# Performance work log

Measured on AMD Instinct MI355X. Metric: run time of the kernel, lower is better.

Reference implementation:

```python
import jax, jax.numpy as jnp
import numpy as np

N_NODES = 50000
N_EDGES = 1600000
D_IN = 64
D_EDGE = 64
DIMS = [128, 128, 128]  # atom_embedding_sizes
N_GRAPHS = 64


def setup_inputs() -> dict:
    key = jax.random.key(0)
    ks = jax.random.split(key, 4 + 4 * len(DIMS))
    inp = {
        "x": jax.random.normal(ks[0], (N_NODES, D_IN), dtype=jnp.float32),
        "edge_index": jax.random.randint(ks[1], (2, N_EDGES), 0, N_NODES),
        "edge_attr": jax.random.uniform(ks[2], (N_EDGES, D_EDGE), dtype=jnp.float32),
        "batch": jnp.sort(jax.random.randint(ks[3], (N_NODES,), 0, N_GRAPHS)),
    }
    in_dim = D_IN
    ki = 4
    for l, out_dim in enumerate(DIMS):
        se = 1.0 / np.sqrt(in_dim + D_EDGE)
        sr = 1.0 / np.sqrt(in_dim)
        inp[f"We{l}"] = jax.random.uniform(ks[ki + 0], (in_dim + D_EDGE, out_dim), jnp.float32, -se, se)
        inp[f"be{l}"] = jnp.zeros((out_dim,), jnp.float32)
        inp[f"Wr{l}"] = jax.random.uniform(ks[ki + 1], (in_dim, out_dim), jnp.float32, -sr, sr)
        inp[f"br{l}"] = jnp.zeros((out_dim,), jnp.float32)
        ki += 2
        in_dim = out_dim
    return inp


def reference(x, edge_index, edge_attr, batch,
              We0, be0, Wr0, br0,
              We1, be1, Wr1, br1,
              We2, be2, Wr2, br2):
    params = [(We0, be0, Wr0, br0), (We1, be1, Wr1, br1), (We2, be2, Wr2, br2)]
    src, dst = edge_index[0], edge_index[1]  # PyG convention: messages flow src -> dst
    for We, be, Wr, br in params:
        # ESAGEConv: message = Linear([x_j || edge_attr]); add-aggregate to dst;
        # root transform Linear(x_i); then ReLU (module activation).
        msg = jnp.concatenate([x[src], edge_attr], axis=-1) @ We + be  # [E, out]
        aggr = jax.ops.segment_sum(msg, dst, num_segments=N_NODES)     # [N, out]
        x = jax.nn.relu(aggr + x @ Wr + br)
    # readout_pooling='add' -> global_add_pool over graph ids
    return jax.ops.segment_sum(x, batch, num_segments=N_GRAPHS)  # [G, out]
```

## Files before the change

### kernel.cpp

```cpp
#include <hip/hip_runtime.h>
#include <hip/hip_bf16.h>
#include <cstdint>

typedef __attribute__((ext_vector_type(8))) short short8v;
typedef __attribute__((ext_vector_type(4))) float f32x4;

__device__ __forceinline__ float4 add4(float4 a, float4 b) {
  return make_float4(a.x + b.x, a.y + b.y, a.z + b.z, a.w + b.w);
}
__device__ __forceinline__ float bf2f(unsigned short u) {
  union { unsigned int i; float f; } v; v.i = ((unsigned int)u) << 16; return v.f;
}
__device__ __forceinline__ unsigned short f2bf(float f) {
  union { float f; unsigned int i; } v; v.f = f;
  unsigned int r = v.i + 0x7fff + ((v.i >> 16) & 1);
  return (unsigned short)(r >> 16);
}


__global__ void count_deg_kernel(const int* __restrict__ dst, int* __restrict__ deg, int E) {
  int i = blockIdx.x * blockDim.x + threadIdx.x;
  if (i < E) atomicAdd(&deg[dst[i]], 1);
}

__global__ void block_sum_kernel(const int* __restrict__ deg, int* __restrict__ bsum, int N) {
  int t = threadIdx.x;
  int i = blockIdx.x * 512 + t;
  int v = (i < N) ? deg[i] : 0;
#pragma unroll
  for (int off = 32; off > 0; off >>= 1) v += __shfl_down(v, off, 64);
  __shared__ int ws[8];
  int lane = t & 63, wid = t >> 6;
  if (lane == 0) ws[wid] = v;
  __syncthreads();
  if (t == 0) {
    int s = 0;
#pragma unroll
    for (int j = 0; j < 8; ++j) s += ws[j];
    bsum[blockIdx.x] = s;
  }
}

__global__ void scan_small_kernel(const int* __restrict__ bsum, int* __restrict__ boffs, int B) {
  int t = threadIdx.x;
  int lane = t & 63, wid = t >> 6;
  int v = (t < B) ? bsum[t] : 0;
  int incl = v;
#pragma unroll
  for (int off = 1; off < 64; off <<= 1) {
    int u = __shfl_up(incl, off, 64);
    if (lane >= off) incl += u;
  }
  __shared__ int ws[2];
  if (lane == 63) ws[wid] = incl;
  __syncthreads();
  int base = (wid == 1) ? ws[0] : 0;
  if (t < B) boffs[t] = base + incl - v;
}

__global__ void ptrs_kernel(const int* __restrict__ deg, const int* __restrict__ boffs,
                            int* __restrict__ ptrs, int N) {
  int t = threadIdx.x;
  int i = blockIdx.x * 512 + t;
  int lane = t & 63, wid = t >> 6;
  int v = (i < N) ? deg[i] : 0;
  int incl = v;
#pragma unroll
  for (int off = 1; off < 64; off <<= 1) {
    int u = __shfl_up(incl, off, 64);
    if (lane >= off) incl += u;
  }
  __shared__ int ws[8];
  if (lane == 63) ws[wid] = incl;
  __syncthreads();
  if (t == 0) {
    int s = 0;
#pragma unroll
    for (int j = 0; j < 8; ++j) { int tmp = ws[j]; ws[j] = s; s += tmp; }
  }
  __syncthreads();
  if (i < N) ptrs[i + 1] = boffs[blockIdx.x] + ws[wid] + incl;
  if (i == 0 && blockIdx.x == 0) ptrs[0] = 0;
}

__global__ void fill_csr_kernel(const int* __restrict__ src, const int* __restrict__ dst,
                                const int* __restrict__ ptrs, int* __restrict__ cnt,
                                int2* __restrict__ csr, int E) {
  int i = blockIdx.x * blockDim.x + threadIdx.x;
  if (i < E) {
    int d = dst[i];
    int pos = ptrs[d] + atomicAdd(&cnt[d], 1);
    csr[pos] = make_int2(src[i], i);
  }
}


__global__ void f2bf_stream_kernel(const float* __restrict__ in, unsigned short* __restrict__ out, int n) {
  int i = (blockIdx.x * blockDim.x + threadIdx.x) * 8;
  if (i < n) {
    float4 v0 = *(const float4*)(in + i);
    float4 v1 = *(const float4*)(in + i + 4);
    short8v o;
    o[0] = (short)f2bf(v0.x); o[1] = (short)f2bf(v0.y);
    o[2] = (short)f2bf(v0.z); o[3] = (short)f2bf(v0.w);
    o[4] = (short)f2bf(v1.x); o[5] = (short)f2bf(v1.y);
    o[6] = (short)f2bf(v1.z); o[7] = (short)f2bf(v1.w);
    *(short8v*)(out + i) = o;
  }
}

__global__ void pack_wt_kernel(const float* __restrict__ We, int rowsE,
                               const float* __restrict__ Wr, int Ktot,
                               unsigned short* __restrict__ Wt) {
  int idx = blockIdx.x * blockDim.x + threadIdx.x;
  if (idx >= 128 * Ktot) return;
  int c = idx / Ktot, k = idx % Ktot;
  float v = (k < rowsE) ? We[(size_t)k * 128 + c] : Wr[(size_t)(k - rowsE) * 128 + c];
  Wt[idx] = f2bf(v);
}


__global__ __launch_bounds__(256) void agg_ea_kernel(
    const int* __restrict__ ptrs, const int2* __restrict__ csr,
    const float* __restrict__ ea, unsigned short* __restrict__ agge, int N) {
  int n = blockIdx.x;
  int t = threadIdx.x;
  int slot = t >> 4, cg = t & 15;
  int s = ptrs[n], e = ptrs[n + 1];
  float4 a0 = make_float4(0, 0, 0, 0), a1 = make_float4(0, 0, 0, 0);
  int i = s + slot;
  for (; i + 16 < e; i += 32) {
    int r0 = csr[i].y, r1 = csr[i + 16].y;
    a0 = add4(a0, *((const float4*)(ea + (size_t)r0 * 64) + cg));
    a1 = add4(a1, *((const float4*)(ea + (size_t)r1 * 64) + cg));
  }
  if (i < e) {
    int r0 = csr[i].y;
    a0 = add4(a0, *((const float4*)(ea + (size_t)r0 * 64) + cg));
  }
  a0 = add4(a0, a1);
  __shared__ float red[16][64];
  *reinterpret_cast<float4*>(&red[slot][cg * 4]) = a0;
  __syncthreads();
  if (t < 64) {
    float sum = 0.f;
#pragma unroll
    for (int r = 0; r < 16; ++r) sum += red[r][t];
    agge[(size_t)n * 64 + t] = f2bf(sum);
  }
}

__global__ __launch_bounds__(256) void agg_bf64_kernel(
    const int* __restrict__ ptrs, const int2* __restrict__ csr,
    const unsigned short* __restrict__ xb, unsigned short* __restrict__ outagg, int N) {
  int n = blockIdx.x;
  int t = threadIdx.x;
  int slot = t >> 3, cg = t & 7;
  int s = ptrs[n], e = ptrs[n + 1];
  float a[8];
#pragma unroll
  for (int j = 0; j < 8; ++j) a[j] = 0.f;
  for (int i = s + slot; i < e; i += 32) {
    int r = csr[i].x;
    short8v v = *(const short8v*)(xb + (size_t)r * 64 + cg * 8);
#pragma unroll
    for (int j = 0; j < 8; ++j) a[j] += bf2f((unsigned short)v[j]);
  }
  __shared__ float red[32][64];
#pragma unroll
  for (int j = 0; j < 8; ++j) red[slot][cg * 8 + j] = a[j];
  __syncthreads();
  if (t < 64) {
    float sum = 0.f;
#pragma unroll
    for (int r = 0; r < 32; ++r) sum += red[r][t];
    outagg[(size_t)n * 64 + t] = f2bf(sum);
  }
}

__global__ __launch_bounds__(256) void agg_bf128_kernel(
    const int* __restrict__ ptrs, const int2* __restrict__ csr,
    const unsigned short* __restrict__ xb, unsigned short* __restrict__ outagg, int N) {
  int n = blockIdx.x;
  int t = threadIdx.x;
  int slot = t >> 4, cg = t & 15;
  int s = ptrs[n], e = ptrs[n + 1];
  float a[8];
#pragma unroll
  for (int j = 0; j < 8; ++j) a[j] = 0.f;
  int i = s + slot;
  for (; i + 16 < e; i += 32) {
    int r0 = csr[i].x, r1 = csr[i + 16].x;
    short8v v0 = *(const short8v*)(xb + (size_t)r0 * 128 + cg * 8);
    short8v v1 = *(const short8v*)(xb + (size_t)r1 * 128 + cg * 8);
#pragma unroll
    for (int j = 0; j < 8; ++j) a[j] += bf2f((unsigned short)v0[j]) + bf2f((unsigned short)v1[j]);
  }
  if (i < e) {
    int r0 = csr[i].x;
    short8v v0 = *(const short8v*)(xb + (size_t)r0 * 128 + cg * 8);
#pragma unroll
    for (int j = 0; j < 8; ++j) a[j] += bf2f((unsigned short)v0[j]);
  }
  __shared__ float red[16][128];
#pragma unroll
  for (int j = 0; j < 8; ++j) red[slot][cg * 8 + j] = a[j];
  __syncthreads();
  if (t < 128) {
    float sum = 0.f;
#pragma unroll
    for (int r = 0; r < 16; ++r) sum += red[r][t];
    outagg[(size_t)n * 128 + t] = f2bf(sum);
  }
}

__global__ __launch_bounds__(256) void gemm_mfma_kernel(
    const unsigned short* __restrict__ A1, int w1, int k1,
    const unsigned short* __restrict__ A2, int w2, int k2,
    const unsigned short* __restrict__ A3, int w3, int k3,
    const unsigned short* __restrict__ Wt, int Ktot,
    const float* __restrict__ be, const float* __restrict__ br,
    const int* __restrict__ deg, unsigned short* __restrict__ out, int N) {
  int t = threadIdx.x;
  int wave = t >> 6, lane = t & 63;
  int rit = lane & 15, kgrp = lane >> 4;
  int n0 = blockIdx.x * 64;
  int arow = n0 + wave * 16 + rit;
  if (arow >= N) arow = N - 1;
  f32x4 acc[8];
#pragma unroll
  for (int c = 0; c < 8; ++c) acc[c] = (f32x4){0.f, 0.f, 0.f, 0.f};

  const unsigned short* As[3] = {A1, A2, A3};
  const int wds[3] = {w1, w2, w3};
  const int ks[3] = {k1, k2, k3};
  int kbase = 0;
  for (int s = 0; s < 3; ++s) {
    const unsigned short* Arow = As[s] + (size_t)arow * wds[s] + kgrp * 8;
    int K = ks[s];
    for (int kk = 0; kk < K; kk += 32) {
      short8v a = *(const short8v*)(Arow + kk);
      int kg = kbase + kk + kgrp * 8;
#pragma unroll
      for (int c = 0; c < 8; ++c) {
        short8v b = *(const short8v*)(Wt + (size_t)(c * 16 + rit) * Ktot + kg);
        acc[c] = __builtin_amdgcn_mfma_f32_16x16x32_bf16(a, b, acc[c], 0, 0, 0);
      }
    }
    kbase += K;
  }

  __shared__ unsigned short st[64][136];
  float dg[4];
#pragma unroll
  for (int r = 0; r < 4; ++r) {
    int n = n0 + wave * 16 + kgrp * 4 + r;
    dg[r] = (float)deg[n < N ? n : N - 1];
  }
#pragma unroll
  for (int c = 0; c < 8; ++c) {
    int col = c * 16 + rit;
    float bev = be[col], brv = br[col];
#pragma unroll
    for (int r = 0; r < 4; ++r) {
      float v = acc[c][r] + dg[r] * bev + brv;
      st[wave * 16 + kgrp * 4 + r][col] = f2bf(fmaxf(v, 0.f));
    }
  }
  __syncthreads();
#pragma unroll
  for (int it = 0; it < 4; ++it) {
    int idx = t + it * 256;
    int row = idx >> 4, cg = idx & 15;
    int n = n0 + row;
    if (n < N)
      *(short8v*)(out + (size_t)n * 128 + cg * 8) = *(const short8v*)(&st[row][cg * 8]);
  }
}

__global__ void pool_kernel(const unsigned short* __restrict__ x, const int* __restrict__ batch,
                            float* __restrict__ out, int N) {
  int n0 = blockIdx.x * 128;
  int c = threadIdx.x;
  if (n0 >= N) return;
  int end = min(n0 + 128, N);
  float acc = 0.f;
  int g = batch[n0];
  for (int n = n0; n < end; ++n) {
    int gn = batch[n];
    if (gn != g) {
      atomicAdd(&out[g * 128 + c], acc);
      acc = 0.f;
      g = gn;
    }
    acc += bf2f(x[(size_t)n * 128 + c]);
  }
  atomicAdd(&out[g * 128 + c], acc);
}


extern "C" void kernel_launch(void* const* d_in, const int* in_sizes, int n_in,
                              void* d_out, int out_size, void* d_ws, size_t ws_size,
                              hipStream_t stream) {
  const float* x_in       = (const float*)d_in[0];
  const int*   edge_index = (const int*)d_in[1];
  const float* edge_attr  = (const float*)d_in[2];
  const int*   batch      = (const int*)d_in[3];
  const float* We0 = (const float*)d_in[4];
  const float* be0 = (const float*)d_in[5];
  const float* Wr0 = (const float*)d_in[6];
  const float* br0 = (const float*)d_in[7];
  const float* We1 = (const float*)d_in[8];
  const float* be1 = (const float*)d_in[9];
  const float* Wr1 = (const float*)d_in[10];
  const float* br1 = (const float*)d_in[11];
  const float* We2 = (const float*)d_in[12];
  const float* be2 = (const float*)d_in[13];
  const float* Wr2 = (const float*)d_in[14];
  const float* br2 = (const float*)d_in[15];

  float* out = (float*)d_out;

  int N = in_sizes[0] / 64;
  int E = in_sizes[1] / 2;
  const int* src = edge_index;
  const int* dst = edge_index + E;

  char* w = (char*)d_ws;
  size_t off = 0;
  auto alloc = [&](size_t bytes) {
    void* p = w + off;
    off += (bytes + 255) & ~(size_t)255;
    return p;
  };
  int* deg   = (int*)alloc((size_t)N * 4);
  int* cnt   = (int*)alloc((size_t)N * 4);
  size_t zero_bytes = off;
  int* ptrs  = (int*)alloc((size_t)(N + 1) * 4);
  int* bsum  = (int*)alloc(128 * 4);
  int* boffs = (int*)alloc(128 * 4);
  int2* csr  = (int2*)alloc((size_t)E * 8);
  unsigned short* x_bf   = (unsigned short*)alloc((size_t)N * 64 * 2);
  unsigned short* aggx64 = (unsigned short*)alloc((size_t)N * 64 * 2);
  unsigned short* agge   = (unsigned short*)alloc((size_t)N * 64 * 2);
  unsigned short* aggx   = (unsigned short*)alloc((size_t)N * 128 * 2);
  unsigned short* xb0    = (unsigned short*)alloc((size_t)N * 128 * 2);
  unsigned short* xb1    = (unsigned short*)alloc((size_t)N * 128 * 2);
  unsigned short* Wt0    = (unsigned short*)alloc((size_t)128 * 192 * 2);
  unsigned short* Wt1    = (unsigned short*)alloc((size_t)128 * 320 * 2);
  unsigned short* Wt2    = (unsigned short*)alloc((size_t)128 * 320 * 2);

  (void)hipMemsetAsync(d_ws, 0, zero_bytes, stream);
  (void)hipMemsetAsync(d_out, 0, (size_t)out_size * sizeof(float), stream);

  int eb = (E + 255) / 256;
  int sb = (N + 511) / 512;
  count_deg_kernel<<<eb, 256, 0, stream>>>(dst, deg, E);
  block_sum_kernel<<<sb, 512, 0, stream>>>(deg, bsum, N);
  scan_small_kernel<<<1, 128, 0, stream>>>(bsum, boffs, sb);
  ptrs_kernel<<<sb, 512, 0, stream>>>(deg, boffs, ptrs, N);
  fill_csr_kernel<<<eb, 256, 0, stream>>>(src, dst, ptrs, cnt, csr, E);

  f2bf_stream_kernel<<<(N * 64 / 8 + 255) / 256, 256, 0, stream>>>(x_in, x_bf, N * 64);
  pack_wt_kernel<<<(128 * 192 + 255) / 256, 256, 0, stream>>>(We0, 128, Wr0, 192, Wt0);
  pack_wt_kernel<<<(128 * 320 + 255) / 256, 256, 0, stream>>>(We1, 192, Wr1, 320, Wt1);
  pack_wt_kernel<<<(128 * 320 + 255) / 256, 256, 0, stream>>>(We2, 192, Wr2, 320, Wt2);

  int gb = (N + 63) / 64;

  agg_ea_kernel<<<N, 256, 0, stream>>>(ptrs, csr, edge_attr, agge, N);
  agg_bf64_kernel<<<N, 256, 0, stream>>>(ptrs, csr, x_bf, aggx64, N);

  gemm_mfma_kernel<<<gb, 256, 0, stream>>>(aggx64, 64, 64, agge, 64, 64, x_bf, 64, 64,
                                           Wt0, 192, be0, br0, deg, xb0, N);
  agg_bf128_kernel<<<N, 256, 0, stream>>>(ptrs, csr, xb0, aggx, N);
  gemm_mfma_kernel<<<gb, 256, 0, stream>>>(aggx, 128, 128, agge, 64, 64, xb0, 128, 128,
                                           Wt1, 320, be1, br1, deg, xb1, N);
  agg_bf128_kernel<<<N, 256, 0, stream>>>(ptrs, csr, xb1, aggx, N);
  gemm_mfma_kernel<<<gb, 256, 0, stream>>>(aggx, 128, 128, agge, 64, 64, xb1, 128, 128,
                                           Wt2, 320, be2, br2, deg, xb0, N);
  pool_kernel<<<(N + 127) / 128, 128, 0, stream>>>(xb0, batch, out, N);
}
```

Measured before the change: 585.2 us.

## Aggregate four destination nodes per block in CSR gather kernels

The edge-attribute, 64-wide and 128-wide aggregation kernels now give each block a contiguous span of four destination nodes instead of one. Threads stride across the combined edge range and route each gathered row into one of four per-node accumulators by comparing its edge index with the node boundaries. The aim is to keep all slots busy when a node has only about 32 edges, and to cut block count and launch overhead. The cost is extra branching, four times the accumulator registers and more shared memory for the reduction. The three weight-packing launches are also merged into one kernel.

```diff
diff --git a/kernel.cpp b/kernel.cpp
--- a/kernel.cpp
+++ b/kernel.cpp
@@ -15,6 +15,32 @@
   union { float f; unsigned int i; } v; v.f = f;
   unsigned int r = v.i + 0x7fff + ((v.i >> 16) & 1);
   return (unsigned short)(r >> 16);
+}
+
+__device__ __forceinline__ void pacc4(int p, int b1, int b2, int b3, float4 v,
+                                      float4& a0, float4& a1, float4& a2, float4& a3) {
+  if (p < b2) { if (p < b1) a0 = add4(a0, v); else a1 = add4(a1, v); }
+  else        { if (p < b3) a2 = add4(a2, v); else a3 = add4(a3, v); }
+}
+__device__ __forceinline__ void pacc8(int p, int b1, int b2, int b3, const float (&f)[8],
+                                      float (&a0)[8], float (&a1)[8], float (&a2)[8], float (&a3)[8]) {
+  if (p < b2) {
+    if (p < b1) {
+#pragma unroll
+      for (int j = 0; j < 8; ++j) a0[j] += f[j];
+    } else {
+#pragma unroll
+      for (int j = 0; j < 8; ++j) a1[j] += f[j];
+    }
+  } else {
+    if (p < b3) {
+#pragma unroll
+      for (int j = 0; j < 8; ++j) a2[j] += f[j];
+    } else {
+#pragma unroll
+      for (int j = 0; j < 8; ++j) a3[j] += f[j];
+    }
+  }
 }
 
 
@@ -109,108 +135,159 @@
   }
 }
 
-__global__ void pack_wt_kernel(const float* __restrict__ We, int rowsE,
-                               const float* __restrict__ Wr, int Ktot,
-                               unsigned short* __restrict__ Wt) {
+__global__ void pack_all_kernel(const float* __restrict__ We0, const float* __restrict__ Wr0,
+                                const float* __restrict__ We1, const float* __restrict__ Wr1,
+                                const float* __restrict__ We2, const float* __restrict__ Wr2,
+                                unsigned short* __restrict__ Wt0, unsigned short* __restrict__ Wt1,
+                                unsigned short* __restrict__ Wt2) {
   int idx = blockIdx.x * blockDim.x + threadIdx.x;
-  if (idx >= 128 * Ktot) return;
-  int c = idx / Ktot, k = idx % Ktot;
+  const float* We; const float* Wr; unsigned short* Wt;
+  int rowsE, Ktot, local;
+  if (idx < 128 * 192) {
+    We = We0; Wr = Wr0; Wt = Wt0; rowsE = 128; Ktot = 192; local = idx;
+  } else if (idx < 128 * 192 + 128 * 320) {
+    We = We1; Wr = Wr1; Wt = Wt1; rowsE = 192; Ktot = 320; local = idx - 128 * 192;
+  } else if (idx < 128 * 192 + 2 * 128 * 320) {
+    We = We2; Wr = Wr2; Wt = Wt2; rowsE = 192; Ktot = 320; local = idx - 128 * 192 - 128 * 320;
+  } else {
+    return;
+  }
+  int c = local / Ktot, k = local % Ktot;
   float v = (k < rowsE) ? We[(size_t)k * 128 + c] : Wr[(size_t)(k - rowsE) * 128 + c];
-  Wt[idx] = f2bf(v);
+  Wt[local] = f2bf(v);
 }
 
 
 __global__ __launch_bounds__(256) void agg_ea_kernel(
     const int* __restrict__ ptrs, const int2* __restrict__ csr,
     const float* __restrict__ ea, unsigned short* __restrict__ agge, int N) {
-  int n = blockIdx.x;
+  int n0 = blockIdx.x * 4;
   int t = threadIdx.x;
   int slot = t >> 4, cg = t & 15;
-  int s = ptrs[n], e = ptrs[n + 1];
-  float4 a0 = make_float4(0, 0, 0, 0), a1 = make_float4(0, 0, 0, 0);
-  int i = s + slot;
-  for (; i + 16 < e; i += 32) {
-    int r0 = csr[i].y, r1 = csr[i + 16].y;
-    a0 = add4(a0, *((const float4*)(ea + (size_t)r0 * 64) + cg));
-    a1 = add4(a1, *((const float4*)(ea + (size_t)r1 * 64) + cg));
-  }
-  if (i < e) {
-    int r0 = csr[i].y;
-    a0 = add4(a0, *((const float4*)(ea + (size_t)r0 * 64) + cg));
-  }
-  a0 = add4(a0, a1);
-  __shared__ float red[16][64];
-  *reinterpret_cast<float4*>(&red[slot][cg * 4]) = a0;
-  __syncthreads();
-  if (t < 64) {
-    float sum = 0.f;
-#pragma unroll
-    for (int r = 0; r < 16; ++r) sum += red[r][t];
-    agge[(size_t)n * 64 + t] = f2bf(sum);
-  }
+  int b0 = ptrs[n0];
+  int b1 = ptrs[min(n0 + 1, N)];
+  int b2 = ptrs[min(n0 + 2, N)];
+  int b3 = ptrs[min(n0 + 3, N)];
+  int b4 = ptrs[min(n0 + 4, N)];
+  float4 z = make_float4(0, 0, 0, 0);
+  float4 a0 = z, a1 = z, a2 = z, a3 = z;
+  int i = b0 + slot;
+  for (; i + 16 < b4; i += 32) {
+    int e0 = csr[i].y, e1 = csr[i + 16].y;
+    float4 v0 = *((const float4*)(ea + (size_t)e0 * 64) + cg);
+    float4 v1 = *((const float4*)(ea + (size_t)e1 * 64) + cg);
+    pacc4(i, b1, b2, b3, v0, a0, a1, a2, a3);
+    pacc4(i + 16, b1, b2, b3, v1, a0, a1, a2, a3);
+  }
+  if (i < b4) {
+    int e0 = csr[i].y;
+    float4 v0 = *((const float4*)(ea + (size_t)e0 * 64) + cg);
+    pacc4(i, b1, b2, b3, v0, a0, a1, a2, a3);
+  }
+  __shared__ float red[16][4][64];
+  *(float4*)&red[slot][0][cg * 4] = a0;
+  *(float4*)&red[slot][1][cg * 4] = a1;
+  *(float4*)&red[slot][2][cg * 4] = a2;
+  *(float4*)&red[slot][3][cg * 4] = a3;
+  __syncthreads();
+  int nd = t >> 6, col = t & 63;
+  float s = 0.f;
+#pragma unroll
+  for (int r = 0; r < 16; ++r) s += red[r][nd][col];
+  int n = n0 + nd;
+  if (n < N) agge[(size_t)n * 64 + col] = f2bf(s);
 }
 
 __global__ __launch_bounds__(256) void agg_bf64_kernel(
     const int* __restrict__ ptrs, const int2* __restrict__ csr,
     const unsigned short* __restrict__ xb, unsigned short* __restrict__ outagg, int N) {
-  int n = blockIdx.x;
+  int n0 = blockIdx.x * 4;
   int t = threadIdx.x;
   int slot = t >> 3, cg = t & 7;
-  int s = ptrs[n], e = ptrs[n + 1];
-  float a[8];
-#pragma unroll
-  for (int j = 0; j < 8; ++j) a[j] = 0.f;
-  for (int i = s + slot; i < e; i += 32) {
+  int b0 = ptrs[n0];
+  int b1 = ptrs[min(n0 + 1, N)];
+  int b2 = ptrs[min(n0 + 2, N)];
+  int b3 = ptrs[min(n0 + 3, N)];
+  int b4 = ptrs[min(n0 + 4, N)];
+  float a0[8], a1[8], a2[8], a3[8];
+#pragma unroll
+  for (int j = 0; j < 8; ++j) { a0[j] = 0.f; a1[j] = 0.f; a2[j] = 0.f; a3[j] = 0.f; }
+  for (int i = b0 + slot; i < b4; i += 32) {
     int r = csr[i].x;
     short8v v = *(const short8v*)(xb + (size_t)r * 64 + cg * 8);
-#pragma unroll
-    for (int j = 0; j < 8; ++j) a[j] += bf2f((unsigned short)v[j]);
-  }
-  __shared__ float red[32][64];
-#pragma unroll
-  for (int j = 0; j < 8; ++j) red[slot][cg * 8 + j] = a[j];
-  __syncthreads();
-  if (t < 64) {
-    float sum = 0.f;
-#pragma unroll
-    for (int r = 0; r < 32; ++r) sum += red[r][t];
-    outagg[(size_t)n * 64 + t] = f2bf(sum);
-  }
+    float f[8];
+#pragma unroll
+    for (int j = 0; j < 8; ++j) f[j] = bf2f((unsigned short)v[j]);
+    pacc8(i, b1, b2, b3, f, a0, a1, a2, a3);
+  }
+  __shared__ float red[32][4][64];
+#pragma unroll
+  for (int j = 0; j < 8; ++j) {
+    red[slot][0][cg * 8 + j] = a0[j];
+    red[slot][1][cg * 8 + j] = a1[j];
+    red[slot][2][cg * 8 + j] = a2[j];
+    red[slot][3][cg * 8 + j] = a3[j];
+  }
+  __syncthreads();
+  int nd = t >> 6, col = t & 63;
+  float s = 0.f;
+#pragma unroll
+  for (int r = 0; r < 32; ++r) s += red[r][nd][col];
+  int n = n0 + nd;
+  if (n < N) outagg[(size_t)n * 64 + col] = f2bf(s);
 }
 
 __global__ __launch_bounds__(256) void agg_bf128_kernel(
     const int* __restrict__ ptrs, const int2* __restrict__ csr,
     const unsigned short* __restrict__ xb, unsigned short* __restrict__ outagg, int N) {
-  int n = blockIdx.x;
+  int n0 = blockIdx.x * 4;
   int t = threadIdx.x;
   int slot = t >> 4, cg = t & 15;
-  int s = ptrs[n], e = ptrs[n + 1];
-  float a[8];
-#pragma unroll
-  for (int j = 0; j < 8; ++j) a[j] = 0.f;
-  int i = s + slot;
-  for (; i + 16 < e; i += 32) {
+  int b0 = ptrs[n0];
+  int b1 = ptrs[min(n0 + 1, N)];
+  int b2 = ptrs[min(n0 + 2, N)];
+  int b3 = ptrs[min(n0 + 3, N)];
+  int b4 = ptrs[min(n0 + 4, N)];
+  float a0[8], a1[8], a2[8], a3[8];
+#pragma unroll
+  for (int j = 0; j < 8; ++j) { a0[j] = 0.f; a1[j] = 0.f; a2[j] = 0.f; a3[j] = 0.f; }
+  int i = b0 + slot;
+  for (; i + 16 < b4; i += 32) {
     int r0 = csr[i].x, r1 = csr[i + 16].x;
     short8v v0 = *(const short8v*)(xb + (size_t)r0 * 128 + cg * 8);
     short8v v1 = *(const short8v*)(xb + (size_t)r1 * 128 + cg * 8);
-#pragma unroll
-    for (int j = 0; j < 8; ++j) a[j] += bf2f((unsigned short)v0[j]) + bf2f((unsigned short)v1[j]);
-  }
-  if (i < e) {
+    float f0[8], f1[8];
+#pragma unroll
+    for (int j = 0; j < 8; ++j) { f0[j] = bf2f((unsigned short)v0[j]); f1[j] = bf2f((unsigned short)v1[j]); }
+    pacc8(i, b1, b2, b3, f0, a0, a1, a2, a3);
+    pacc8(i + 16, b1, b2, b3, f1, a0, a1, a2, a3);
+  }
+  if (i < b4) {
     int r0 = csr[i].x;
     short8v v0 = *(const short8v*)(xb + (size_t)r0 * 128 + cg * 8);
-#pragma unroll
-    for (int j = 0; j < 8; ++j) a[j] += bf2f((unsigned short)v0[j]);
-  }
-  __shared__ float red[16][128];
-#pragma unroll
-  for (int j = 0; j < 8; ++j) red[slot][cg * 8 + j] = a[j];
-  __syncthreads();
-  if (t < 128) {
-    float sum = 0.f;
-#pragma unroll
-    for (int r = 0; r < 16; ++r) sum += red[r][t];
-    outagg[(size_t)n * 128 + t] = f2bf(sum);
+    float f0[8];
+#pragma unroll
+    for (int j = 0; j < 8; ++j) f0[j] = bf2f((unsigned short)v0[j]);
+    pacc8(i, b1, b2, b3, f0, a0, a1, a2, a3);
+  }
+  __shared__ float red[16][4][128];
+#pragma unroll
+  for (int j = 0; j < 8; ++j) {
+    red[slot][0][cg * 8 + j] = a0[j];
+    red[slot][1][cg * 8 + j] = a1[j];
+    red[slot][2][cg * 8 + j] = a2[j];
+    red[slot][3][cg * 8 + j] = a3[j];
+  }
+  __syncthreads();
+#pragma unroll
+  for (int rr = 0; rr < 2; ++rr) {
+    int idx = t + rr * 256;
+    int nd = idx >> 7, col = idx & 127;
+    float s = 0.f;
+#pragma unroll
+    for (int r = 0; r < 16; ++r) s += red[r][nd][col];
+    int n = n0 + nd;
+    if (n < N) outagg[(size_t)n * 128 + col] = f2bf(s);
   }
 }
 
@@ -362,21 +439,24 @@
   fill_csr_kernel<<<eb, 256, 0, stream>>>(src, dst, ptrs, cnt, csr, E);
 
   f2bf_stream_kernel<<<(N * 64 / 8 + 255) / 256, 256, 0, stream>>>(x_in, x_bf, N * 64);
-  pack_wt_kernel<<<(128 * 192 + 255) / 256, 256, 0, stream>>>(We0, 128, Wr0, 192, Wt0);
-  pack_wt_kernel<<<(128 * 320 + 255) / 256, 256, 0, stream>>>(We1, 192, Wr1, 320, Wt1);
-  pack_wt_kernel<<<(128 * 320 + 255) / 256, 256, 0, stream>>>(We2, 192, Wr2, 320, Wt2);
+  {
+    int total = 128 * 192 + 2 * 128 * 320;
+    pack_all_kernel<<<(total + 255) / 256, 256, 0, stream>>>(We0, Wr0, We1, Wr1, We2, Wr2,
+                                                             Wt0, Wt1, Wt2);
+  }
 
   int gb = (N + 63) / 64;
-
-  agg_ea_kernel<<<N, 256, 0, stream>>>(ptrs, csr, edge_attr, agge, N);
-  agg_bf64_kernel<<<N, 256, 0, stream>>>(ptrs, csr, x_bf, aggx64, N);
+  int ab = (N + 3) / 4;
+
+  agg_ea_kernel<<<ab, 256, 0, stream>>>(ptrs, csr, edge_attr, agge, N);
+  agg_bf64_kernel<<<ab, 256, 0, stream>>>(ptrs, csr, x_bf, aggx64, N);
 
   gemm_mfma_kernel<<<gb, 256, 0, stream>>>(aggx64, 64, 64, agge, 64, 64, x_bf, 64, 64,
                                            Wt0, 192, be0, br0, deg, xb0, N);
-  agg_bf128_kernel<<<N, 256, 0, stream>>>(ptrs, csr, xb0, aggx, N);
+  agg_bf128_kernel<<<ab, 256, 0, stream>>>(ptrs, csr, xb0, aggx, N);
   gemm_mfma_kernel<<<gb, 256, 0, stream>>>(aggx, 128, 128, agge, 64, 64, xb0, 128, 128,
                                            Wt1, 320, be1, br1, deg, xb1, N);
-  agg_bf128_kernel<<<N, 256, 0, stream>>>(ptrs, csr, xb1, aggx, N);
+  agg_bf128_kernel<<<ab, 256, 0, stream>>>(ptrs, csr, xb1, aggx, N);
   gemm_mfma_kernel<<<gb, 256, 0, stream>>>(aggx, 128, 128, agge, 64, 64, xb1, 128, 128,
                                            Wt2, 320, be2, br2, deg, xb0, N);
   pool_kernel<<<(N + 127) / 128, 128, 0, stream>>>(xb0, batch, out, N);
```

Result: slower. 1.176 ms (+101.0%).

## Aggregate one node per wavefront with shuffle reductions instead of per-block LDS

Applied to the files above, without the earlier changes.

The CSR gather-aggregation kernels now give each node one 64-lane wavefront, four nodes per block, instead of a full 256-thread block per node. The partial sums are combined with xor shuffles, so the shared-memory reduction and __syncthreads are gone. This targets the idle threads and sync overhead of a whole block working on an average of about 32 edges. The three weight-packing launches are also merged into one kernel to cut launch overhead. Each wave now carries fewer edges in flight, so memory-level parallelism per node is lower.

```diff
diff --git a/kernel.cpp b/kernel.cpp
--- a/kernel.cpp
+++ b/kernel.cpp
@@ -3,6 +3,7 @@
 #include <cstdint>
 
 typedef __attribute__((ext_vector_type(8))) short short8v;
+typedef __attribute__((ext_vector_type(4))) short short4v;
 typedef __attribute__((ext_vector_type(4))) float f32x4;
 
 __device__ __forceinline__ float4 add4(float4 a, float4 b) {
@@ -15,6 +16,16 @@
   union { float f; unsigned int i; } v; v.f = f;
   unsigned int r = v.i + 0x7fff + ((v.i >> 16) & 1);
   return (unsigned short)(r >> 16);
+}
+__device__ __forceinline__ float4 shflx4(float4 a, int m) {
+  return make_float4(__shfl_xor(a.x, m, 64), __shfl_xor(a.y, m, 64),
+                     __shfl_xor(a.z, m, 64), __shfl_xor(a.w, m, 64));
+}
+__device__ __forceinline__ void acc8(float4& lo, float4& hi, short8v v) {
+  lo.x += bf2f((unsigned short)v[0]); lo.y += bf2f((unsigned short)v[1]);
+  lo.z += bf2f((unsigned short)v[2]); lo.w += bf2f((unsigned short)v[3]);
+  hi.x += bf2f((unsigned short)v[4]); hi.y += bf2f((unsigned short)v[5]);
+  hi.z += bf2f((unsigned short)v[6]); hi.w += bf2f((unsigned short)v[7]);
 }
 
 
@@ -109,108 +120,115 @@
   }
 }
 
-__global__ void pack_wt_kernel(const float* __restrict__ We, int rowsE,
-                               const float* __restrict__ Wr, int Ktot,
-                               unsigned short* __restrict__ Wt) {
+__global__ void pack_all_kernel(const float* __restrict__ We0, const float* __restrict__ Wr0,
+                                const float* __restrict__ We1, const float* __restrict__ Wr1,
+                                const float* __restrict__ We2, const float* __restrict__ Wr2,
+                                unsigned short* __restrict__ Wt0, unsigned short* __restrict__ Wt1,
+                                unsigned short* __restrict__ Wt2) {
   int idx = blockIdx.x * blockDim.x + threadIdx.x;
-  if (idx >= 128 * Ktot) return;
-  int c = idx / Ktot, k = idx % Ktot;
+  const float* We; const float* Wr; unsigned short* Wt;
+  int rowsE, Ktot, local;
+  if (idx < 128 * 192) {
+    We = We0; Wr = Wr0; Wt = Wt0; rowsE = 128; Ktot = 192; local = idx;
+  } else if (idx < 128 * 192 + 128 * 320) {
+    We = We1; Wr = Wr1; Wt = Wt1; rowsE = 192; Ktot = 320; local = idx - 128 * 192;
+  } else if (idx < 128 * 192 + 2 * 128 * 320) {
+    We = We2; Wr = Wr2; Wt = Wt2; rowsE = 192; Ktot = 320; local = idx - 128 * 192 - 128 * 320;
+  } else {
+    return;
+  }
+  int c = local / Ktot, k = local % Ktot;
   float v = (k < rowsE) ? We[(size_t)k * 128 + c] : Wr[(size_t)(k - rowsE) * 128 + c];
-  Wt[idx] = f2bf(v);
+  Wt[local] = f2bf(v);
 }
 
 
 __global__ __launch_bounds__(256) void agg_ea_kernel(
     const int* __restrict__ ptrs, const int2* __restrict__ csr,
     const float* __restrict__ ea, unsigned short* __restrict__ agge, int N) {
-  int n = blockIdx.x;
-  int t = threadIdx.x;
-  int slot = t >> 4, cg = t & 15;
+  int t = threadIdx.x;
+  int n = blockIdx.x * 4 + (t >> 6);
+  if (n >= N) return;
+  int lane = t & 63;
+  int slot = lane >> 4, cg = lane & 15;
   int s = ptrs[n], e = ptrs[n + 1];
   float4 a0 = make_float4(0, 0, 0, 0), a1 = make_float4(0, 0, 0, 0);
   int i = s + slot;
-  for (; i + 16 < e; i += 32) {
-    int r0 = csr[i].y, r1 = csr[i + 16].y;
-    a0 = add4(a0, *((const float4*)(ea + (size_t)r0 * 64) + cg));
-    a1 = add4(a1, *((const float4*)(ea + (size_t)r1 * 64) + cg));
-  }
-  if (i < e) {
-    int r0 = csr[i].y;
-    a0 = add4(a0, *((const float4*)(ea + (size_t)r0 * 64) + cg));
-  }
+  for (; i + 4 < e; i += 8) {
+    int e0 = csr[i].y, e1 = csr[i + 4].y;
+    a0 = add4(a0, *((const float4*)(ea + (size_t)e0 * 64) + cg));
+    a1 = add4(a1, *((const float4*)(ea + (size_t)e1 * 64) + cg));
+  }
+  if (i < e) a0 = add4(a0, *((const float4*)(ea + (size_t)csr[i].y * 64) + cg));
   a0 = add4(a0, a1);
-  __shared__ float red[16][64];
-  *reinterpret_cast<float4*>(&red[slot][cg * 4]) = a0;
-  __syncthreads();
-  if (t < 64) {
-    float sum = 0.f;
-#pragma unroll
-    for (int r = 0; r < 16; ++r) sum += red[r][t];
-    agge[(size_t)n * 64 + t] = f2bf(sum);
+  a0 = add4(a0, shflx4(a0, 16));
+  a0 = add4(a0, shflx4(a0, 32));
+  if (slot == 0) {
+    short4v o;
+    o[0] = (short)f2bf(a0.x); o[1] = (short)f2bf(a0.y);
+    o[2] = (short)f2bf(a0.z); o[3] = (short)f2bf(a0.w);
+    *(short4v*)(agge + (size_t)n * 64 + cg * 4) = o;
   }
 }
 
 __global__ __launch_bounds__(256) void agg_bf64_kernel(
     const int* __restrict__ ptrs, const int2* __restrict__ csr,
     const unsigned short* __restrict__ xb, unsigned short* __restrict__ outagg, int N) {
-  int n = blockIdx.x;
-  int t = threadIdx.x;
-  int slot = t >> 3, cg = t & 7;
+  int t = threadIdx.x;
+  int n = blockIdx.x * 4 + (t >> 6);
+  if (n >= N) return;
+  int lane = t & 63;
+  int slot = lane >> 3, cg = lane & 7;
   int s = ptrs[n], e = ptrs[n + 1];
-  float a[8];
-#pragma unroll
-  for (int j = 0; j < 8; ++j) a[j] = 0.f;
-  for (int i = s + slot; i < e; i += 32) {
-    int r = csr[i].x;
-    short8v v = *(const short8v*)(xb + (size_t)r * 64 + cg * 8);
-#pragma unroll
-    for (int j = 0; j < 8; ++j) a[j] += bf2f((unsigned short)v[j]);
-  }
-  __shared__ float red[32][64];
-#pragma unroll
-  for (int j = 0; j < 8; ++j) red[slot][cg * 8 + j] = a[j];
-  __syncthreads();
-  if (t < 64) {
-    float sum = 0.f;
-#pragma unroll
-    for (int r = 0; r < 32; ++r) sum += red[r][t];
-    outagg[(size_t)n * 64 + t] = f2bf(sum);
+  float4 lo0 = make_float4(0, 0, 0, 0), hi0 = make_float4(0, 0, 0, 0);
+  float4 lo1 = make_float4(0, 0, 0, 0), hi1 = make_float4(0, 0, 0, 0);
+  int i = s + slot;
+  for (; i + 8 < e; i += 16) {
+    acc8(lo0, hi0, *(const short8v*)(xb + (size_t)csr[i].x * 64 + cg * 8));
+    acc8(lo1, hi1, *(const short8v*)(xb + (size_t)csr[i + 8].x * 64 + cg * 8));
+  }
+  if (i < e) acc8(lo0, hi0, *(const short8v*)(xb + (size_t)csr[i].x * 64 + cg * 8));
+  lo0 = add4(lo0, lo1); hi0 = add4(hi0, hi1);
+  lo0 = add4(lo0, shflx4(lo0, 8));  hi0 = add4(hi0, shflx4(hi0, 8));
+  lo0 = add4(lo0, shflx4(lo0, 16)); hi0 = add4(hi0, shflx4(hi0, 16));
+  lo0 = add4(lo0, shflx4(lo0, 32)); hi0 = add4(hi0, shflx4(hi0, 32));
+  if (slot == 0) {
+    short8v o;
+    o[0] = (short)f2bf(lo0.x); o[1] = (short)f2bf(lo0.y);
+    o[2] = (short)f2bf(lo0.z); o[3] = (short)f2bf(lo0.w);
+    o[4] = (short)f2bf(hi0.x); o[5] = (short)f2bf(hi0.y);
+    o[6] = (short)f2bf(hi0.z); o[7] = (short)f2bf(hi0.w);
+    *(short8v*)(outagg + (size_t)n * 64 + cg * 8) = o;
   }
 }
 
 __global__ __launch_bounds__(256) void agg_bf128_kernel(
     const int* __restrict__ ptrs, const int2* __restrict__ csr,
     const unsigned short* __restrict__ xb, unsigned short* __restrict__ outagg, int N) {
-  int n = blockIdx.x;
-  int t = threadIdx.x;
-  int slot = t >> 4, cg = t & 15;
+  int t = threadIdx.x;
+  int n = blockIdx.x * 4 + (t >> 6);
+  if (n >= N) return;
+  int lane = t & 63;
+  int slot = lane >> 4, cg = lane & 15;
   int s = ptrs[n], e = ptrs[n + 1];
-  float a[8];
-#pragma unroll
-  for (int j = 0; j < 8; ++j) a[j] = 0.f;
+  float4 lo0 = make_float4(0, 0, 0, 0), hi0 = make_float4(0, 0, 0, 0);
+  float4 lo1 = make_float4(0, 0, 0, 0), hi1 = make_float4(0, 0, 0, 0);
   int i = s + slot;
-  for (; i + 16 < e; i += 32) {
-    int r0 = csr[i].x, r1 = csr[i + 16].x;
-    short8v v0 = *(const short8v*)(xb + (size_t)r0 * 128 + cg * 8);
-    short8v v1 = *(const short8v*)(xb + (size_t)r1 * 128 + cg * 8);
-#pragma unroll
-    for (int j = 0; j < 8; ++j) a[j] += bf2f((unsigned short)v0[j]) + bf2f((unsigned short)v1[j]);
-  }
-  if (i < e) {
-    int r0 = csr[i].x;
-    short8v v0 = *(const short8v*)(xb + (size_t)r0 * 128 + cg * 8);
-#pragma unroll
-    for (int j = 0; j < 8; ++j) a[j] += bf2f((unsigned short)v0[j]);
-  }
-  __shared__ float red[16][128];
-#pragma unroll
-  for (int j = 0; j < 8; ++j) red[slot][cg * 8 + j] = a[j];
-  __syncthreads();
-  if (t < 128) {
-    float sum = 0.f;
-#pragma unroll
-    for (int r = 0; r < 16; ++r) sum += red[r][t];
-    outagg[(size_t)n * 128 + t] = f2bf(sum);
+  for (; i + 4 < e; i += 8) {
+    acc8(lo0, hi0, *(const short8v*)(xb + (size_t)csr[i].x * 128 + cg * 8));
+    acc8(lo1, hi1, *(const short8v*)(xb + (size_t)csr[i + 4].x * 128 + cg * 8));
+  }
+  if (i < e) acc8(lo0, hi0, *(const short8v*)(xb + (size_t)csr[i].x * 128 + cg * 8));
+  lo0 = add4(lo0, lo1); hi0 = add4(hi0, hi1);
+  lo0 = add4(lo0, shflx4(lo0, 16)); hi0 = add4(hi0, shflx4(hi0, 16));
+  lo0 = add4(lo0, shflx4(lo0, 32)); hi0 = add4(hi0, shflx4(hi0, 32));
+  if (slot == 0) {
+    short8v o;
+    o[0] = (short)f2bf(lo0.x); o[1] = (short)f2bf(lo0.y);
+    o[2] = (short)f2bf(lo0.z); o[3] = (short)f2bf(lo0.w);
+    o[4] = (short)f2bf(hi0.x); o[5] = (short)f2bf(hi0.y);
+    o[6] = (short)f2bf(hi0.z); o[7] = (short)f2bf(hi0.w);
+    *(short8v*)(outagg + (size_t)n * 128 + cg * 8) = o;
   }
 }
 
@@ -362,21 +380,24 @@
   fill_csr_kernel<<<eb, 256, 0, stream>>>(src, dst, ptrs, cnt, csr, E);
 
   f2bf_stream_kernel<<<(N * 64 / 8 + 255) / 256, 256, 0, stream>>>(x_in, x_bf, N * 64);
-  pack_wt_kernel<<<(128 * 192 + 255) / 256, 256, 0, stream>>>(We0, 128, Wr0, 192, Wt0);
-  pack_wt_kernel<<<(128 * 320 + 255) / 256, 256, 0, stream>>>(We1, 192, Wr1, 320, Wt1);
-  pack_wt_kernel<<<(128 * 320 + 255) / 256, 256, 0, stream>>>(We2, 192, Wr2, 320, Wt2);
+  {
+    int total = 128 * 192 + 2 * 128 * 320;
+    pack_all_kernel<<<(total + 255) / 256, 256, 0, stream>>>(We0, Wr0, We1, Wr1, We2, Wr2,
+                                                             Wt0, Wt1, Wt2);
+  }
 
   int gb = (N + 63) / 64;
-
-  agg_ea_kernel<<<N, 256, 0, stream>>>(ptrs, csr, edge_attr, agge, N);
-  agg_bf64_kernel<<<N, 256, 0, stream>>>(ptrs, csr, x_bf, aggx64, N);
+  int ab = (N + 3) / 4;
+
+  agg_ea_kernel<<<ab, 256, 0, stream>>>(ptrs, csr, edge_attr, agge, N);
+  agg_bf64_kernel<<<ab, 256, 0, stream>>>(ptrs, csr, x_bf, aggx64, N);
 
   gemm_mfma_kernel<<<gb, 256, 0, stream>>>(aggx64, 64, 64, agge, 64, 64, x_bf, 64, 64,
                                            Wt0, 192, be0, br0, deg, xb0, N);
-  agg_bf128_kernel<<<N, 256, 0, stream>>>(ptrs, csr, xb0, aggx, N);
+  agg_bf128_kernel<<<ab, 256, 0, stream>>>(ptrs, csr, xb0, aggx, N);
   gemm_mfma_kernel<<<gb, 256, 0, stream>>>(aggx, 128, 128, agge, 64, 64, xb0, 128, 128,
                                            Wt1, 320, be1, br1, deg, xb1, N);
-  agg_bf128_kernel<<<N, 256, 0, stream>>>(ptrs, csr, xb1, aggx, N);
+  agg_bf128_kernel<<<ab, 256, 0, stream>>>(ptrs, csr, xb1, aggx, N);
   gemm_mfma_kernel<<<gb, 256, 0, stream>>>(aggx, 128, 128, agge, 64, 64, xb1, 128, 128,
                                            Wt2, 320, be2, br2, deg, xb0, N);
   pool_kernel<<<(N + 127) / 128, 128, 0, stream>>>(xb0, batch, out, N);
```

Result: faster. 539.9 us (-7.7%).
